# Kernel tuning notes

Hardware: AMD Instinct MI355X
Metric: run time of the kernel (lower is better)

## Reference

```python
import jax, jax.numpy as jnp
import numpy as np

THRESHOLD = 0.35      # overlap_thresh
NEGPOS_RATIO = 7
VAR0, VAR1 = 0.1, 0.2  # self.variance


def make_priors():
    # Standard RetinaFace 640x640 anchor grid -> 16800 priors (cx, cy, w, h)
    img = 640
    steps = [8, 16, 32]
    min_sizes = [[16, 32], [64, 128], [256, 512]]
    out = []
    for step, ms in zip(steps, min_sizes):
        f = img // step
        ii, jj = np.meshgrid(np.arange(f), np.arange(f), indexing="ij")
        cx = ((jj + 0.5) * step / img).ravel().astype(np.float32)
        cy = ((ii + 0.5) * step / img).ravel().astype(np.float32)
        for m in ms:
            s = np.full_like(cx, m / img)
            out.append(np.stack([cx, cy, s, s], axis=-1))
    return jnp.asarray(np.concatenate(out, axis=0), dtype=jnp.float32)


def jaccard(a, b):
    # a: [O,4] point-form gt boxes, b: [P,4] point-form priors -> IoU [O,P]
    lt = jnp.maximum(a[:, None, :2], b[None, :, :2])
    rb = jnp.minimum(a[:, None, 2:], b[None, :, 2:])
    wh = jnp.clip(rb - lt, 0.0)
    inter = wh[..., 0] * wh[..., 1]
    area_a = ((a[:, 2] - a[:, 0]) * (a[:, 3] - a[:, 1]))[:, None]
    area_b = ((b[:, 2] - b[:, 0]) * (b[:, 3] - b[:, 1]))[None, :]
    return inter / (area_a + area_b - inter)


def setup_inputs() -> dict:
    key = jax.random.key(0)
    ks = jax.random.split(key, 7)
    B, P, O = 64, 16800, 64
    loc_data = jax.random.normal(ks[0], (B, P, 4), jnp.float32)
    conf_data = jax.random.normal(ks[1], (B, P, 2), jnp.float32)
    landm_data = jax.random.normal(ks[2], (B, P, 10), jnp.float32)
    priors = make_priors()
    # targets: [B, O, 15] = [xmin ymin xmax ymax | 10 landmark coords | label]
    c = jax.random.uniform(ks[3], (B, O, 2), minval=0.15, maxval=0.85)
    wh = jax.random.uniform(ks[4], (B, O, 2), minval=0.05, maxval=0.3)
    boxes = jnp.concatenate([jnp.clip(c - wh / 2, 1e-3, 0.999),
                             jnp.clip(c + wh / 2, 1e-3, 0.999)], axis=-1)
    landms = jax.random.uniform(ks[5], (B, O, 10))
    lab = jnp.where(jax.random.uniform(ks[6], (B, O, 1)) < 0.8, 1.0, -1.0)
    targets = jnp.concatenate([boxes, landms, lab], axis=-1).astype(jnp.float32)
    return {"loc_data": loc_data, "conf_data": conf_data,
            "landm_data": landm_data, "priors": priors, "targets": targets}


def _smooth_l1(x):
    ax = jnp.abs(x)
    return jnp.where(ax < 1.0, 0.5 * ax * ax, ax - 0.5)


def reference(loc_data, conf_data, landm_data, priors, targets):
    B, P, C = conf_data.shape
    O = targets.shape[1]
    priors_pf = jnp.concatenate([priors[:, :2] - priors[:, 2:] * 0.5,
                                 priors[:, :2] + priors[:, 2:] * 0.5], axis=1)

    def match_one(t):
        truths = t[:, :4]
        landms = t[:, 4:14]
        labels = t[:, 14].astype(jnp.int32)
        ov = jaccard(truths, priors_pf)               # [O,P]
        bp_ov = ov.max(axis=1)                         # best prior per truth
        bp_idx = jnp.argmax(ov, axis=1)
        valid = bp_ov >= 0.2                           # RetinaFace gt filter
        bt_ov = ov.max(axis=0)                         # best truth per prior
        bt_idx = jnp.argmax(ov, axis=0)
        # index_fill_(best_prior_idx, 2) for valid gts, ensure best prior kept
        bt_ov = bt_ov.at[bp_idx].set(jnp.where(valid, 2.0, bt_ov[bp_idx]))
        bt_idx = bt_idx.at[bp_idx].set(jnp.arange(O))
        matched = truths[bt_idx]                       # [P,4] point form
        conf = labels[bt_idx]
        conf = jnp.where(bt_ov < THRESHOLD, 0, conf)
        # encode loc target
        g_cxcy = ((matched[:, :2] + matched[:, 2:]) * 0.5 - priors[:, :2]) / (VAR0 * priors[:, 2:])
        g_wh = jnp.log((matched[:, 2:] - matched[:, :2]) / priors[:, 2:]) / VAR1
        loc = jnp.concatenate([g_cxcy, g_wh], axis=1)
        # encode landmark target (5 points)
        ml = landms[bt_idx].reshape(P, 5, 2)
        lm = ((ml - priors[:, None, :2]) / (VAR0 * priors[:, None, 2:])).reshape(P, 10)
        any_valid = jnp.any(valid)                     # early-return branch of match()
        return (jnp.where(any_valid, loc, 0.0),
                jnp.where(any_valid, conf, 0),
                jnp.where(any_valid, lm, 0.0))

    loc_t, conf_t, landm_t = jax.vmap(match_one)(targets)
    loc_t = jax.lax.stop_gradient(loc_t)       # targets built from .data in torch
    landm_t = jax.lax.stop_gradient(landm_t)

    # landmark loss over conf_t > 0
    pos1 = conf_t > 0
    N1 = jnp.maximum(pos1.sum().astype(jnp.float32), 1.0)
    loss_landm = jnp.sum(jnp.where(pos1[..., None], _smooth_l1(landm_data - landm_t), 0.0))

    # localization loss over conf_t != 0 (labels -1 and 1 both positive)
    pos = conf_t != 0
    conf_t1 = jnp.where(pos, 1, conf_t)        # conf_t[pos] = 1 -> values in {0,1}
    loss_l = jnp.sum(jnp.where(pos[..., None], _smooth_l1(loc_data - loc_t), 0.0))

    # hard negative mining
    lse = jax.nn.logsumexp(conf_data, axis=2)                       # [B,P]
    picked = jnp.take_along_axis(conf_data, conf_t1[..., None], axis=2)[..., 0]
    ce_all = lse - picked                                            # per-anchor CE
    rank_score = jnp.where(pos, 0.0, ce_all)
    loss_idx = jnp.argsort(-rank_score, axis=1)
    idx_rank = jnp.argsort(loss_idx, axis=1)
    num_pos = pos.sum(axis=1, keepdims=True)
    num_neg = jnp.minimum(NEGPOS_RATIO * num_pos, P - 1)
    neg = idx_rank < num_neg
    union = pos | neg
    loss_c = jnp.sum(jnp.where(union, ce_all, 0.0))

    N = jnp.maximum(num_pos.sum().astype(jnp.float32), 1.0)
    return loss_l / N, loss_c / N, loss_landm / N1
```

## Files before the change

### kernel.cpp

```cpp
#include <hip/hip_runtime.h>
#include <math.h>

#define B 64
#define P 16800
#define O 64
#define THRESH 0.35f
#define VALID_T 0.2f
#define HB 2048
#define HSHIFT 21
#define AREA_M 0.34f
#define CCAP 4096
#define MULT 2
#define RPB 2
#define CHB (MULT * 256)
#define NB2 ((P + CHB - 1) / CHB)
#define KD1B ((B / RPB) * NB2)
#define KB2B (B * O / 4)

__device__ __forceinline__ float smooth_l1(float x) {
    float ax = fabsf(x);
    return ax < 1.f ? 0.5f * ax * ax : ax - 0.5f;
}
__device__ __forceinline__ float lse2(float c0, float c1) {
    float m = fmaxf(c0, c1);
    return m + __logf(__expf(c0 - m) + __expf(c1 - m));
}
__device__ __forceinline__ void iou_upd(float4 t, float area_a,
                                        float px1, float py1, float px2, float py2,
                                        float area_b,
                                        float& bnum, float& bden, int& bio, int o) {
    float w = fmaxf(fminf(t.z, px2) - fmaxf(t.x, px1), 0.f);
    float h = fmaxf(fminf(t.w, py2) - fmaxf(t.y, py1), 0.f);
    float inter = w * h;
    float den = area_a + area_b - inter;
    if (inter * bden > bnum * den) { bnum = inter; bden = den; bio = o; }
}
__device__ __forceinline__ float wave_sum(float v) {
#pragma unroll
    for (int s = 32; s > 0; s >>= 1) v += __shfl_down(v, s, 64);
    return v;
}
__device__ __forceinline__ int wave_sum_i(int v) {
#pragma unroll
    for (int s = 32; s > 0; s >>= 1) v += __shfl_down(v, s, 64);
    return v;
}
__device__ __forceinline__ float wave_min(float v) {
#pragma unroll
    for (int s = 32; s > 0; s >>= 1) v = fminf(v, __shfl_xor(v, s, 64));
    return v;
}
__device__ __forceinline__ float wave_max(float v) {
#pragma unroll
    for (int s = 32; s > 0; s >>= 1) v = fmaxf(v, __shfl_xor(v, s, 64));
    return v;
}
__device__ __forceinline__ int wave_sufscan(int v, int lane) {
#pragma unroll
    for (int s = 1; s < 64; s <<= 1) {
        int o = __shfl_down(v, s, 64);
        if (lane + s < 64) v += o;
    }
    return v;
}
__device__ __forceinline__ void wave0_select(const int* h, int nb, int k,
                                             int* s_bin, int* s_kk, int tid) {
    if (tid >= 64) return;
    int lane = tid;
    int bpl = (nb + 63) >> 6;
    int b0 = lane * bpl;
    int s = 0;
    for (int i = 0; i < bpl; ++i) { int bb = b0 + i; if (bb < nb) s += h[bb]; }
    int suf = wave_sufscan(s, lane);
    int sufn = __shfl_down(suf, 1, 64);
    if (lane == 63) sufn = 0;
    if (suf >= k && sufn < k) {
        int cum = sufn;
        for (int i = bpl - 1; i >= 0; --i) {
            int bb = b0 + i; if (bb >= nb) continue;
            int hv = h[bb];
            if (cum + hv >= k) { *s_bin = bb; *s_kk = k - cum; break; }
            cum += hv;
        }
    }
}

__global__ void __launch_bounds__(256) kMain(
        const float* __restrict__ loc_data,
        const float* __restrict__ landm_data, const float* __restrict__ priors,
        const float* __restrict__ targets,
        unsigned char* __restrict__ pflag,
        int* __restrict__ num_pos,
        float* __restrict__ gsum, int* __restrict__ np1_tot,
        unsigned long long* __restrict__ bp_final) {
    if (blockIdx.x >= KD1B) {
        int pair = (blockIdx.x - KD1B) * 4 + (threadIdx.x >> 6);
        int lane = threadIdx.x & 63;
        int o = pair & (O - 1);
        int b = pair >> 6;
        const float* tt = &targets[(b * O + o) * 15];
        float tx1 = tt[0], ty1 = tt[1], tx2 = tt[2], ty2 = tt[3];
        float area_a = (tx2 - tx1) * (ty2 - ty1);
        float4 tb = make_float4(tx1, ty1, tx2, ty2);
        float bn = 0.f, bd = 1.f;
        unsigned bp = 0u;
        const int fs[6]   = {80, 80, 40, 40, 20, 20};
        const int ms[6]   = {16, 32, 64, 128, 256, 512};
        const int base[6] = {0, 6400, 12800, 14400, 16000, 16400};
#pragma unroll
        for (int c = 0; c < 6; ++c) {
            int f = fs[c];
            float inv = (float)f;
            float h = (float)ms[c] * (0.5f / 640.f);
            int j0 = (int)floorf((tx1 - h) * inv - 0.5f) - 1; if (j0 < 0) j0 = 0;
            int j1 = (int)ceilf((tx2 + h) * inv - 0.5f) + 1;  if (j1 > f - 1) j1 = f - 1;
            int i0 = (int)floorf((ty1 - h) * inv - 0.5f) - 1; if (i0 < 0) i0 = 0;
            int i1 = (int)ceilf((ty2 + h) * inv - 0.5f) + 1;  if (i1 > f - 1) i1 = f - 1;
            if (j1 < j0 || i1 < i0) continue;
            int nj = j1 - j0 + 1;
            int n = (i1 - i0 + 1) * nj;
            float rcp_nj = 1.0f / (float)nj;
            for (int idx = lane; idx < n; idx += 64) {
                int ii = (int)((float)idx * rcp_nj);
                int jj = idx - ii * nj;
                if (jj < 0) { ii--; jj += nj; } else if (jj >= nj) { ii++; jj -= nj; }
                int p = base[c] + (i0 + ii) * f + (j0 + jj);
                float4 q = ((const float4*)priors)[p];
                float px1 = q.x - q.z * 0.5f, py1 = q.y - q.w * 0.5f;
                float px2 = q.x + q.z * 0.5f, py2 = q.y + q.w * 0.5f;
                float areab = (px2 - px1) * (py2 - py1);
                float w = fmaxf(fminf(tb.z, px2) - fmaxf(tb.x, px1), 0.f);
                float hh = fmaxf(fminf(tb.w, py2) - fmaxf(tb.y, py1), 0.f);
                float inter = w * hh;
                float den = area_a + areab - inter;
                float l = bn * den, r = inter * bd;
                if (r > l) { bn = inter; bd = den; bp = (unsigned)p; }
            }
        }
#pragma unroll
        for (int s = 32; s > 0; s >>= 1) {
            float no = __shfl_xor(bn, s, 64), dd = __shfl_xor(bd, s, 64);
            unsigned po = __shfl_xor(bp, s, 64);
            float l = bn * dd, r = no * bd;
            bool take = (r > l) || (r == l && po < bp);
            if (take) { bn = no; bd = dd; bp = po; }
        }
        if (lane == 0) {
            float iou = bn / bd;
            bp_final[b * O + o] = ((unsigned long long)__float_as_uint(iou) << 32)
                                | (unsigned)(0xFFFFFFFFu - bp);
        }
        return;
    }
    int blk = blockIdx.x % NB2;
    int rp = blockIdx.x / NB2;
    int p0 = blk * CHB;
    __shared__ float traw[O * 15];
    __shared__ float4 t4[O];
    __shared__ float ta[O], lab[O];
    __shared__ float wredf[2][4];
    __shared__ int wredi[2][4];
    int tid = threadIdx.x;
    int wid = tid >> 6, lid = tid & 63;
    float px1[MULT], py1[MULT], px2[MULT], py2[MULT], areab[MULT];
    float4 pr4[MULT];
    bool act[MULT];
    float cbx1[MULT], cby1[MULT], cbx2[MULT], cby2[MULT], camn[MULT], camx[MULT];
#pragma unroll
    for (int mi = 0; mi < MULT; ++mi) {
        int p = p0 + mi * 256 + tid;
        act[mi] = (p < P);
        int pc = act[mi] ? p : (P - 1);
        float4 q = ((const float4*)priors)[pc];
        pr4[mi] = q;
        px1[mi] = q.x - q.z * 0.5f; py1[mi] = q.y - q.w * 0.5f;
        px2[mi] = q.x + q.z * 0.5f; py2[mi] = q.y + q.w * 0.5f;
        areab[mi] = (px2[mi] - px1[mi]) * (py2[mi] - py1[mi]);
        cbx1[mi] = wave_min(px1[mi]); cby1[mi] = wave_min(py1[mi]);
        cbx2[mi] = wave_max(px2[mi]); cby2[mi] = wave_max(py2[mi]);
        camn[mi] = wave_min(areab[mi]); camx[mi] = wave_max(areab[mi]);
    }
    for (int r = 0; r < RPB; ++r) {
        int b = rp * RPB + r;
        __syncthreads();
        if (tid < O * 15 / 4)
            ((float4*)traw)[tid] = ((const float4*)(targets + (size_t)b * O * 15))[tid];
        __syncthreads();
        if (tid < 64) {
            const float* tr = &traw[tid * 15];
            float a0 = tr[0], a1 = tr[1], a2 = tr[2], a3 = tr[3];
            t4[tid] = make_float4(a0, a1, a2, a3);
            ta[tid] = (a2 - a0) * (a3 - a1);
            lab[tid] = tr[14];
        }
        __syncthreads();
        float4 tl = t4[lid];
        float Aal = ta[lid];
        unsigned long long mk[MULT];
#pragma unroll
        for (int mi = 0; mi < MULT; ++mi) {
            bool pass = (fminf(tl.z, cbx2[mi]) - fmaxf(tl.x, cbx1[mi]) > 0.f) &&
                        (fminf(tl.w, cby2[mi]) - fmaxf(tl.y, cby1[mi]) > 0.f) &&
                        (Aal >= AREA_M * camn[mi]) && (camx[mi] >= AREA_M * Aal);
            mk[mi] = __ballot(pass);
        }
        float bnum[MULT], bden[MULT]; int bi[MULT];
#pragma unroll
        for (int mi = 0; mi < MULT; ++mi) {
            bnum[mi] = 0.f; bden[mi] = 1.f; bi[mi] = 0;
            unsigned long long mm = mk[mi];
            float Ap = areab[mi];
            while (mm) {
                int o = __ffsll(mm) - 1;
                mm &= mm - 1;
                float4 t = t4[o];
                float Aa = ta[o];
                if (Aa >= AREA_M * Ap && Ap >= AREA_M * Aa)
                    iou_upd(t, Aa, px1[mi], py1[mi], px2[mi], py2[mi], Ap,
                            bnum[mi], bden[mi], bi[mi], o);
            }
        }
        float ll = 0.f, llm = 0.f;
        int cp = 0, cp1 = 0;
#pragma unroll
        for (int mi = 0; mi < MULT; ++mi) {
            if (!act[mi]) continue;
            int p = p0 + mi * 256 + tid;
            float best = bnum[mi] / bden[mi];
            int conf = (best >= THRESH) ? (int)lab[bi[mi]] : 0;
            bool pos = conf != 0;
            pflag[(size_t)b * P + p] = pos ? 1 : 0;
            if (pos) {
                cp++;
                int ti = bi[mi];
                float cx = pr4[mi].x, cy = pr4[mi].y, sw = pr4[mi].z, sh = pr4[mi].w;
                float4 t = t4[ti];
                float gx = ((t.x + t.z) * 0.5f - cx) / (0.1f * sw);
                float gy = ((t.y + t.w) * 0.5f - cy) / (0.1f * sh);
                float gw = logf((t.z - t.x) / sw) / 0.2f;
                float gh = logf((t.w - t.y) / sh) / 0.2f;
                const float* ld = &loc_data[(size_t)(b * P + p) * 4];
                ll += smooth_l1(ld[0] - gx) + smooth_l1(ld[1] - gy) +
                      smooth_l1(ld[2] - gw) + smooth_l1(ld[3] - gh);
                if (conf > 0) {
                    cp1++;
                    const float* lmd = &landm_data[(size_t)(b * P + p) * 10];
                    const float* lmt = &traw[ti * 15 + 4];
                    for (int k5 = 0; k5 < 5; ++k5) {
                        float lx = (lmt[k5 * 2 + 0] - cx) / (0.1f * sw);
                        float ly = (lmt[k5 * 2 + 1] - cy) / (0.1f * sh);
                        llm += smooth_l1(lmd[k5 * 2 + 0] - lx) + smooth_l1(lmd[k5 * 2 + 1] - ly);
                    }
                }
            }
        }
        float s_ll = wave_sum(ll), s_llm = wave_sum(llm);
        int s_cp = wave_sum_i(cp), s_cp1 = wave_sum_i(cp1);
        if (lid == 0) {
            wredf[0][wid] = s_ll; wredf[1][wid] = s_llm;
            wredi[0][wid] = s_cp; wredi[1][wid] = s_cp1;
        }
        __syncthreads();
        if (tid == 0) {
            float ll_t = wredf[0][0] + wredf[0][1] + wredf[0][2] + wredf[0][3];
            float llm_t = wredf[1][0] + wredf[1][1] + wredf[1][2] + wredf[1][3];
            int cp_t = wredi[0][0] + wredi[0][1] + wredi[0][2] + wredi[0][3];
            int cp1_t = wredi[1][0] + wredi[1][1] + wredi[1][2] + wredi[1][3];
            if (ll_t != 0.f)  atomicAdd(&gsum[0], ll_t);
            if (llm_t != 0.f) atomicAdd(&gsum[1], llm_t);
            if (cp_t)  atomicAdd(&num_pos[b], cp_t);
            if (cp1_t) atomicAdd(np1_tot, cp1_t);
        }
    }
}

__global__ void __launch_bounds__(1024) kTail(
        const float* __restrict__ priors, const float* __restrict__ targets,
        const float* __restrict__ loc_data, const float* __restrict__ conf_data,
        const float* __restrict__ landm_data,
        const unsigned long long* __restrict__ bp_final,
        const unsigned char* __restrict__ pflag,
        const int* __restrict__ num_pos,
        float* __restrict__ gsum, int* __restrict__ np1_tot, int* __restrict__ np_tot,
        float* __restrict__ lossc_tot, int* __restrict__ done,
        float* __restrict__ out) {
    __shared__ __align__(16) unsigned lrow[P];
    __shared__ int lh4[4][HB];
    __shared__ float4 t4[O];
    __shared__ float ta[O], lab[O];
    __shared__ int sp[O];
    __shared__ int hist2[256];
    __shared__ unsigned lcand[CCAP];
    __shared__ int s_np, s_bin0, s_kk0, s_bin, s_kk, s_cnt;
    __shared__ float wredf[16];
    __shared__ int wredi[16];
    __shared__ float s_cepw[16];
    __shared__ float s_sumgt;
    int* lh = lh4[0];

    int b = blockIdx.x;
    int tid = threadIdx.x;
    for (int i = tid; i < 4 * HB; i += 1024) lh4[0][i] = 0;
    if (tid == 0) s_cnt = 0;
    int p = 0, v = 0;
    if (tid < O) {
        const float* tt = &targets[(b * O + tid) * 15];
        float4 tj = make_float4(tt[0], tt[1], tt[2], tt[3]);
        t4[tid] = tj;
        ta[tid] = (tj.z - tj.x) * (tj.w - tj.y);
        lab[tid] = tt[14];
        unsigned long long kpk = bp_final[b * O + tid];
        p = (int)(0xFFFFFFFFu - (unsigned)(kpk & 0xFFFFFFFFu));
        float iou = __uint_as_float((unsigned)(kpk >> 32));
        v = (iou >= VALID_T) ? 1 : 0;
        sp[tid] = p;
    }
    __syncthreads();
    const float4* c4 = (const float4*)(conf_data + (size_t)b * P * 2);
    const uchar4* f4v = (const uchar4*)(pflag + (size_t)b * P);
    int* lhm = lh4[tid >> 8];
    float cep = 0.f;
    for (int i = tid; i < P / 4; i += 1024) {
        float4 a = c4[2 * i];
        float4 c = c4[2 * i + 1];
        uchar4 fl = f4v[i];
        float l0 = lse2(a.x, a.y), l1 = lse2(a.z, a.w);
        float l2 = lse2(c.x, c.y), l3 = lse2(c.z, c.w);
        bool q0 = fl.x != 0, q1 = fl.y != 0, q2 = fl.z != 0, q3 = fl.w != 0;
        float ce0 = l0 - (q0 ? a.y : a.x);
        float ce1 = l1 - (q1 ? a.w : a.z);
        float ce2 = l2 - (q2 ? c.y : c.x);
        float ce3 = l3 - (q3 ? c.w : c.z);
        if (q0) cep += ce0;
        if (q1) cep += ce1;
        if (q2) cep += ce2;
        if (q3) cep += ce3;
        unsigned u0 = __float_as_uint(q0 ? 0.f : ce0);
        unsigned u1 = __float_as_uint(q1 ? 0.f : ce1);
        unsigned u2 = __float_as_uint(q2 ? 0.f : ce2);
        unsigned u3 = __float_as_uint(q3 ? 0.f : ce3);
        ((uint4*)lrow)[i] = make_uint4(u0, u1, u2, u3);
        atomicAdd(&lhm[u0 >> HSHIFT], 1);
        atomicAdd(&lhm[u1 >> HSHIFT], 1);
        atomicAdd(&lhm[u2 >> HSHIFT], 1);
        atomicAdd(&lhm[u3 >> HSHIFT], 1);
    }
    {
        float sc = wave_sum(cep);
        if ((tid & 63) == 0) s_cepw[tid >> 6] = sc;
    }
    __syncthreads();
    for (int i = tid; i < HB; i += 1024)
        lh[i] = lh4[0][i] + lh4[1][i] + lh4[2][i] + lh4[3][i];
    __syncthreads();
    int dnp = 0, dn1 = 0;
    float dll = 0.f, dllm = 0.f, dce = 0.f;
    if (tid < O) {
        int j = tid;
        bool winner = true;
        for (int jj = j + 1; jj < O; ++jj)
            if (sp[jj] == p) { winner = false; break; }
        if (winner) {
            float4 q = ((const float4*)priors)[p];
            float px1 = q.x - q.z * 0.5f, py1 = q.y - q.w * 0.5f;
            float px2 = q.x + q.z * 0.5f, py2 = q.y + q.w * 0.5f;
            float areab = (px2 - px1) * (py2 - py1);
            float bnum = 0.f, bden = 1.f; int bi = 0;
            for (int o = 0; o < O; ++o) {
                float Aa = ta[o];
                if (Aa >= AREA_M * areab && areab >= AREA_M * Aa)
                    iou_upd(t4[o], Aa, px1, py1, px2, py2, areab, bnum, bden, bi, o);
            }
            float best = bnum / bden;
            float ov_new = v ? 2.0f : best;
            int conf_old = (best >= THRESH) ? (int)lab[bi] : 0;
            int conf_new = (ov_new >= THRESH) ? (int)lab[j] : 0;
            float2 c01 = ((const float2*)conf_data)[b * P + p];
            float c0 = c01.x, c1 = c01.y;
            float lse = lse2(c0, c1);
            bool po = conf_old != 0, pn = conf_new != 0;
            float ceo = lse - (po ? c1 : c0), cen = lse - (pn ? c1 : c0);
            float rvo = po ? 0.f : ceo, rvn = pn ? 0.f : cen;
            if (__float_as_uint(rvo) != __float_as_uint(rvn)) {
                lrow[p] = __float_as_uint(rvn);
                int bo = __float_as_uint(rvo) >> HSHIFT, bn = __float_as_uint(rvn) >> HSHIFT;
                if (bo != bn) { atomicAdd(&lh[bn], 1); atomicAdd(&lh[bo], -1); }
            }
            const float* ld = &loc_data[(size_t)(b * P + p) * 4];
            auto enc_ll = [&](int ti) -> float {
                float4 t = t4[ti];
                float gx = ((t.x + t.z) * 0.5f - q.x) / (0.1f * q.z);
                float gy = ((t.y + t.w) * 0.5f - q.y) / (0.1f * q.w);
                float gw = logf((t.z - t.x) / q.z) / 0.2f;
                float gh = logf((t.w - t.y) / q.w) / 0.2f;
                return smooth_l1(ld[0] - gx) + smooth_l1(ld[1] - gy) +
                       smooth_l1(ld[2] - gw) + smooth_l1(ld[3] - gh);
            };
            if (po) dll -= enc_ll(bi);
            if (pn) dll += enc_ll(j);
            dce = (pn ? cen : 0.f) - (po ? ceo : 0.f);
            dnp = (int)pn - (int)po;
            const float* lmd = &landm_data[(size_t)(b * P + p) * 10];
            auto enc_lm = [&](int ti) -> float {
                const float* lmt = &targets[(b * O + ti) * 15 + 4];
                float sum = 0.f;
                for (int k5 = 0; k5 < 5; ++k5) {
                    float lx = (lmt[k5 * 2 + 0] - q.x) / (0.1f * q.z);
                    float ly = (lmt[k5 * 2 + 1] - q.y) / (0.1f * q.w);
                    sum += smooth_l1(lmd[k5 * 2 + 0] - lx) + smooth_l1(lmd[k5 * 2 + 1] - ly);
                }
                return sum;
            };
            if (conf_old > 0) dllm -= enc_lm(bi);
            if (conf_new > 0) dllm += enc_lm(j);
            dn1 = (int)(conf_new > 0) - (int)(conf_old > 0);
        }
    }
    float pce_reg = 0.f;
    if (tid < 64) {
        float r_ll = wave_sum(dll), r_lm = wave_sum(dllm), r_ce = wave_sum(dce);
        int r_np = wave_sum_i(dnp), r_n1 = wave_sum_i(dn1);
        if (tid == 0) {
            if (r_ll != 0.f) atomicAdd(&gsum[0], r_ll);
            if (r_lm != 0.f) atomicAdd(&gsum[1], r_lm);
            float cep_tot = 0.f;
            for (int i = 0; i < 16; ++i) cep_tot += s_cepw[i];
            pce_reg = cep_tot + r_ce;
            int np = num_pos[b] + r_np;
            s_np = np;
            atomicAdd(np_tot, np);
            if (r_n1) atomicAdd(np1_tot, r_n1);
        }
    }
    __syncthreads();
    int k = s_np * 7;
    if (k > P - 1) k = P - 1;
    if (tid == 0) { s_bin0 = (k <= 0) ? -1 : 0; s_kk0 = (k <= 0) ? 0 : k; }
    if (k > 0) wave0_select(lh, HB, k, &s_bin0, &s_kk0, tid);
    __syncthreads();
    int bin = s_bin0;
    int kk0 = s_kk0;
    float topk_b = 0.f;
    if (bin >= 0) {
        if (tid < 256) hist2[tid] = 0;
        __syncthreads();
        unsigned lo_bound = ((unsigned)(bin + 1)) << HSHIFT;
        float sumgt = 0.f;
        for (int i = tid; i < P / 4; i += 1024) {
            uint4 u4 = ((const uint4*)lrow)[i];
#define TAIL_H(u) { if ((u) >= lo_bound) sumgt += __uint_as_float(u); \
                    else if (((u) >> HSHIFT) == (unsigned)bin) { \
                        int idx = atomicAdd(&s_cnt, 1); \
                        if (idx < CCAP) lcand[idx] = (u); \
                        atomicAdd(&hist2[((u) >> 13) & 255], 1); } }
            TAIL_H(u4.x) TAIL_H(u4.y) TAIL_H(u4.z) TAIL_H(u4.w)
#undef TAIL_H
        }
        float sg = wave_sum(sumgt);
        if ((tid & 63) == 0) wredf[tid >> 6] = sg;
        __syncthreads();
        if (tid == 0) {
            float t = 0.f;
            for (int i = 0; i < 16; ++i) t += wredf[i];
            s_sumgt = t;
        }
        wave0_select(hist2, 256, kk0, &s_bin, &s_kk, tid);
        __syncthreads();
        unsigned pref = (((unsigned)bin) << HSHIFT) | (((unsigned)s_bin) << 13);
        unsigned resolved = (0xFFFFFFFFu << HSHIFT) | (255u << 13);
        int kk = s_kk;
        int m = s_cnt;
        bool useG = (m > CCAP);
        for (int pass = 0; pass < 2; ++pass) {
            int sh = pass == 0 ? 5 : 0;
            int nb = pass == 0 ? 256 : 32;
            if (tid < nb) hist2[tid] = 0;
            __syncthreads();
            if (!useG) {
                for (int i = tid; i < m; i += 1024) {
                    unsigned u = lcand[i];
                    if ((u & resolved) == pref) atomicAdd(&hist2[(u >> sh) & (nb - 1)], 1);
                }
            } else {
                for (int pp = tid; pp < P; pp += 1024) {
                    unsigned u = lrow[pp];
                    if ((u & resolved) == pref) atomicAdd(&hist2[(u >> sh) & (nb - 1)], 1);
                }
            }
            __syncthreads();
            wave0_select(hist2, nb, kk, &s_bin, &s_kk, tid);
            __syncthreads();
            pref |= ((unsigned)s_bin) << sh;
            resolved |= (unsigned)(nb - 1) << sh;
            kk = s_kk;
        }
        float tv = __uint_as_float(pref);
        float sumS = 0.f; int cntS = 0;
        for (int pp = tid; pp < P; pp += 1024) {
            unsigned u = lrow[pp];
            if ((u >> HSHIFT) == (unsigned)bin) {
                float val = __uint_as_float(u);
                if (val > tv) { sumS += val; cntS++; }
            }
        }
        float s2 = wave_sum(sumS); int c2 = wave_sum_i(cntS);
        if ((tid & 63) == 0) { wredf[tid >> 6] = s2; wredi[tid >> 6] = c2; }
        __syncthreads();
        if (tid == 0) {
            float st = 0.f; int ct = 0;
            for (int i = 0; i < 16; ++i) { st += wredf[i]; ct += wredi[i]; }
            topk_b = s_sumgt + st + (float)(kk0 - ct) * tv;
        }
    }
    if (tid == 0) {
        atomicAdd(lossc_tot, pce_reg + topk_b);
        __threadfence();
        int old = atomicAdd(done, 1);
        if (old == B - 1) {
            float g0 = atomicAdd(&gsum[0], 0.f);
            float g1 = atomicAdd(&gsum[1], 0.f);
            float lc = atomicAdd(lossc_tot, 0.f);
            int np = atomicAdd(np_tot, 0);
            int n1 = atomicAdd(np1_tot, 0);
            float N = fmaxf((float)np, 1.f);
            float N1 = fmaxf((float)n1, 1.f);
            out[0] = g0 / N;
            out[1] = lc / N;
            out[2] = g1 / N1;
        }
    }
}

extern "C" void kernel_launch(void* const* d_in, const int* in_sizes, int n_in,
                              void* d_out, int out_size, void* d_ws, size_t ws_size,
                              hipStream_t stream) {
    const float* loc_data   = (const float*)d_in[0];
    const float* conf_data  = (const float*)d_in[1];
    const float* landm_data = (const float*)d_in[2];
    const float* priors     = (const float*)d_in[3];
    const float* targets    = (const float*)d_in[4];
    float* out = (float*)d_out;

    char* ws = (char*)d_ws;
    size_t off = 0;
    auto alloc = [&](size_t bytes) -> void* {
        void* pp = ws + off;
        off += (bytes + 255) & ~(size_t)255;
        return pp;
    };
    unsigned char* pflag = (unsigned char*)alloc((size_t)B * P);
    unsigned long long* bp_final = (unsigned long long*)alloc((size_t)B * O * 8);
    size_t acc_bytes = (size_t)(B * 4 + 64);
    char* acc = (char*)alloc(acc_bytes);
    int*   num_pos      = (int*)acc;
    float* gsum         = (float*)(acc + B * 4);
    int*   np1_tot      = (int*)(acc + B * 4 + 8);
    int*   np_tot       = (int*)(acc + B * 4 + 12);
    float* lossc_tot    = (float*)(acc + B * 4 + 16);
    int*   done         = (int*)(acc + B * 4 + 20);

    hipMemsetAsync(acc, 0, acc_bytes, stream);
    kMain<<<dim3(KD1B + KB2B), dim3(256), 0, stream>>>(loc_data, landm_data,
                                                       priors, targets, pflag,
                                                       num_pos, gsum, np1_tot,
                                                       bp_final);
    kTail<<<dim3(B), dim3(1024), 0, stream>>>(priors, targets, loc_data, conf_data,
                                              landm_data, bp_final, pflag,
                                              num_pos, gsum, np1_tot, np_tot,
                                              lossc_tot, done, out);
}
```

Baseline: 165.6 us.

## Move per-GT best-prior search into tail kernel and privatize tail histograms

The per-ground-truth best-prior IoU search moves out of extra blocks in the main kernel and into the start of the per-batch tail kernel. Each wave computes four GTs and writes the result to shared memory, so the global bp_final buffer and its round trip go away. The tail's candidate collection now uses wave-aggregated ballot atomics on the shared counter, and the radix-select histograms are split into four per-256-thread copies to reduce atomic contention. The trade-off is that the tail kernel, which runs only 64 blocks, now does the IoU search serially before its main work, which may lengthen the critical path.

```diff
diff --git a/kernel.cpp b/kernel.cpp
--- a/kernel.cpp
+++ b/kernel.cpp
@@ -15,7 +15,6 @@
 #define CHB (MULT * 256)
 #define NB2 ((P + CHB - 1) / CHB)
 #define KD1B ((B / RPB) * NB2)
-#define KB2B (B * O / 4)
 
 __device__ __forceinline__ float smooth_l1(float x) {
     float ax = fabsf(x);
@@ -91,67 +90,7 @@
         const float* __restrict__ targets,
         unsigned char* __restrict__ pflag,
         int* __restrict__ num_pos,
-        float* __restrict__ gsum, int* __restrict__ np1_tot,
-        unsigned long long* __restrict__ bp_final) {
-    if (blockIdx.x >= KD1B) {
-        int pair = (blockIdx.x - KD1B) * 4 + (threadIdx.x >> 6);
-        int lane = threadIdx.x & 63;
-        int o = pair & (O - 1);
-        int b = pair >> 6;
-        const float* tt = &targets[(b * O + o) * 15];
-        float tx1 = tt[0], ty1 = tt[1], tx2 = tt[2], ty2 = tt[3];
-        float area_a = (tx2 - tx1) * (ty2 - ty1);
-        float4 tb = make_float4(tx1, ty1, tx2, ty2);
-        float bn = 0.f, bd = 1.f;
-        unsigned bp = 0u;
-        const int fs[6]   = {80, 80, 40, 40, 20, 20};
-        const int ms[6]   = {16, 32, 64, 128, 256, 512};
-        const int base[6] = {0, 6400, 12800, 14400, 16000, 16400};
-#pragma unroll
-        for (int c = 0; c < 6; ++c) {
-            int f = fs[c];
-            float inv = (float)f;
-            float h = (float)ms[c] * (0.5f / 640.f);
-            int j0 = (int)floorf((tx1 - h) * inv - 0.5f) - 1; if (j0 < 0) j0 = 0;
-            int j1 = (int)ceilf((tx2 + h) * inv - 0.5f) + 1;  if (j1 > f - 1) j1 = f - 1;
-            int i0 = (int)floorf((ty1 - h) * inv - 0.5f) - 1; if (i0 < 0) i0 = 0;
-            int i1 = (int)ceilf((ty2 + h) * inv - 0.5f) + 1;  if (i1 > f - 1) i1 = f - 1;
-            if (j1 < j0 || i1 < i0) continue;
-            int nj = j1 - j0 + 1;
-            int n = (i1 - i0 + 1) * nj;
-            float rcp_nj = 1.0f / (float)nj;
-            for (int idx = lane; idx < n; idx += 64) {
-                int ii = (int)((float)idx * rcp_nj);
-                int jj = idx - ii * nj;
-                if (jj < 0) { ii--; jj += nj; } else if (jj >= nj) { ii++; jj -= nj; }
-                int p = base[c] + (i0 + ii) * f + (j0 + jj);
-                float4 q = ((const float4*)priors)[p];
-                float px1 = q.x - q.z * 0.5f, py1 = q.y - q.w * 0.5f;
-                float px2 = q.x + q.z * 0.5f, py2 = q.y + q.w * 0.5f;
-                float areab = (px2 - px1) * (py2 - py1);
-                float w = fmaxf(fminf(tb.z, px2) - fmaxf(tb.x, px1), 0.f);
-                float hh = fmaxf(fminf(tb.w, py2) - fmaxf(tb.y, py1), 0.f);
-                float inter = w * hh;
-                float den = area_a + areab - inter;
-                float l = bn * den, r = inter * bd;
-                if (r > l) { bn = inter; bd = den; bp = (unsigned)p; }
-            }
-        }
-#pragma unroll
-        for (int s = 32; s > 0; s >>= 1) {
-            float no = __shfl_xor(bn, s, 64), dd = __shfl_xor(bd, s, 64);
-            unsigned po = __shfl_xor(bp, s, 64);
-            float l = bn * dd, r = no * bd;
-            bool take = (r > l) || (r == l && po < bp);
-            if (take) { bn = no; bd = dd; bp = po; }
-        }
-        if (lane == 0) {
-            float iou = bn / bd;
-            bp_final[b * O + o] = ((unsigned long long)__float_as_uint(iou) << 32)
-                                | (unsigned)(0xFFFFFFFFu - bp);
-        }
-        return;
-    }
+        float* __restrict__ gsum, int* __restrict__ np1_tot) {
     int blk = blockIdx.x % NB2;
     int rp = blockIdx.x / NB2;
     int p0 = blk * CHB;
@@ -278,7 +217,6 @@
         const float* __restrict__ priors, const float* __restrict__ targets,
         const float* __restrict__ loc_data, const float* __restrict__ conf_data,
         const float* __restrict__ landm_data,
-        const unsigned long long* __restrict__ bp_final,
         const unsigned char* __restrict__ pflag,
         const int* __restrict__ num_pos,
         float* __restrict__ gsum, int* __restrict__ np1_tot, int* __restrict__ np_tot,
@@ -286,10 +224,12 @@
         float* __restrict__ out) {
     __shared__ __align__(16) unsigned lrow[P];
     __shared__ int lh4[4][HB];
+    __shared__ unsigned long long s_bpk[O];
     __shared__ float4 t4[O];
     __shared__ float ta[O], lab[O];
     __shared__ int sp[O];
     __shared__ int hist2[256];
+    __shared__ int hist2r[4][256];
     __shared__ unsigned lcand[CCAP];
     __shared__ int s_np, s_bin0, s_kk0, s_bin, s_kk, s_cnt;
     __shared__ float wredf[16];
@@ -300,8 +240,66 @@
 
     int b = blockIdx.x;
     int tid = threadIdx.x;
+    int lane = tid & 63;
+    int wv = tid >> 6;
     for (int i = tid; i < 4 * HB; i += 1024) lh4[0][i] = 0;
     if (tid == 0) s_cnt = 0;
+    for (int it = 0; it < 4; ++it) {
+        int o = wv + it * 16;
+        const float* tt = &targets[(b * O + o) * 15];
+        float tx1 = tt[0], ty1 = tt[1], tx2 = tt[2], ty2 = tt[3];
+        float area_a = (tx2 - tx1) * (ty2 - ty1);
+        float4 tb = make_float4(tx1, ty1, tx2, ty2);
+        float bn = 0.f, bd = 1.f;
+        unsigned bp = 0u;
+        const int fs[6]   = {80, 80, 40, 40, 20, 20};
+        const int ms[6]   = {16, 32, 64, 128, 256, 512};
+        const int base[6] = {0, 6400, 12800, 14400, 16000, 16400};
+#pragma unroll
+        for (int c = 0; c < 6; ++c) {
+            int f = fs[c];
+            float inv = (float)f;
+            float h = (float)ms[c] * (0.5f / 640.f);
+            int j0 = (int)floorf((tx1 - h) * inv - 0.5f) - 1; if (j0 < 0) j0 = 0;
+            int j1 = (int)ceilf((tx2 + h) * inv - 0.5f) + 1;  if (j1 > f - 1) j1 = f - 1;
+            int i0 = (int)floorf((ty1 - h) * inv - 0.5f) - 1; if (i0 < 0) i0 = 0;
+            int i1 = (int)ceilf((ty2 + h) * inv - 0.5f) + 1;  if (i1 > f - 1) i1 = f - 1;
+            if (j1 < j0 || i1 < i0) continue;
+            int nj = j1 - j0 + 1;
+            int n = (i1 - i0 + 1) * nj;
+            float rcp_nj = 1.0f / (float)nj;
+            for (int idx = lane; idx < n; idx += 64) {
+                int ii = (int)((float)idx * rcp_nj);
+                int jj = idx - ii * nj;
+                if (jj < 0) { ii--; jj += nj; } else if (jj >= nj) { ii++; jj -= nj; }
+                int p = base[c] + (i0 + ii) * f + (j0 + jj);
+                float4 q = ((const float4*)priors)[p];
+                float px1 = q.x - q.z * 0.5f, py1 = q.y - q.w * 0.5f;
+                float px2 = q.x + q.z * 0.5f, py2 = q.y + q.w * 0.5f;
+                float areab = (px2 - px1) * (py2 - py1);
+                float w = fmaxf(fminf(tb.z, px2) - fmaxf(tb.x, px1), 0.f);
+                float hh = fmaxf(fminf(tb.w, py2) - fmaxf(tb.y, py1), 0.f);
+                float inter = w * hh;
+                float den = area_a + areab - inter;
+                float l = bn * den, r = inter * bd;
+                if (r > l) { bn = inter; bd = den; bp = (unsigned)p; }
+            }
+        }
+#pragma unroll
+        for (int s = 32; s > 0; s >>= 1) {
+            float no = __shfl_xor(bn, s, 64), dd = __shfl_xor(bd, s, 64);
+            unsigned po = __shfl_xor(bp, s, 64);
+            float l = bn * dd, r = no * bd;
+            bool take = (r > l) || (r == l && po < bp);
+            if (take) { bn = no; bd = dd; bp = po; }
+        }
+        if (lane == 0) {
+            float iou = bn / bd;
+            s_bpk[o] = ((unsigned long long)__float_as_uint(iou) << 32)
+                     | (unsigned)(0xFFFFFFFFu - bp);
+        }
+    }
+    __syncthreads();
     int p = 0, v = 0;
     if (tid < O) {
         const float* tt = &targets[(b * O + tid) * 15];
@@ -309,13 +307,12 @@
         t4[tid] = tj;
         ta[tid] = (tj.z - tj.x) * (tj.w - tj.y);
         lab[tid] = tt[14];
-        unsigned long long kpk = bp_final[b * O + tid];
+        unsigned long long kpk = s_bpk[tid];
         p = (int)(0xFFFFFFFFu - (unsigned)(kpk & 0xFFFFFFFFu));
         float iou = __uint_as_float((unsigned)(kpk >> 32));
         v = (iou >= VALID_T) ? 1 : 0;
         sp[tid] = p;
     }
-    __syncthreads();
     const float4* c4 = (const float4*)(conf_data + (size_t)b * P * 2);
     const uchar4* f4v = (const uchar4*)(pflag + (size_t)b * P);
     int* lhm = lh4[tid >> 8];
@@ -347,7 +344,7 @@
     }
     {
         float sc = wave_sum(cep);
-        if ((tid & 63) == 0) s_cepw[tid >> 6] = sc;
+        if (lane == 0) s_cepw[wv] = sc;
     }
     __syncthreads();
     for (int i = tid; i < HB; i += 1024)
@@ -442,28 +439,45 @@
     int kk0 = s_kk0;
     float topk_b = 0.f;
     if (bin >= 0) {
-        if (tid < 256) hist2[tid] = 0;
+        for (int i = tid; i < 4 * 256; i += 1024) hist2r[0][i] = 0;
         __syncthreads();
         unsigned lo_bound = ((unsigned)(bin + 1)) << HSHIFT;
+        int* h2 = hist2r[tid >> 8];
         float sumgt = 0.f;
         for (int i = tid; i < P / 4; i += 1024) {
             uint4 u4 = ((const uint4*)lrow)[i];
-#define TAIL_H(u) { if ((u) >= lo_bound) sumgt += __uint_as_float(u); \
-                    else if (((u) >> HSHIFT) == (unsigned)bin) { \
-                        int idx = atomicAdd(&s_cnt, 1); \
-                        if (idx < CCAP) lcand[idx] = (u); \
-                        atomicAdd(&hist2[((u) >> 13) & 255], 1); } }
-            TAIL_H(u4.x) TAIL_H(u4.y) TAIL_H(u4.z) TAIL_H(u4.w)
-#undef TAIL_H
+#define TAIL_E(u) { \
+            bool gt = (u) >= lo_bound; \
+            bool inb = !gt && (((u) >> HSHIFT) == (unsigned)bin); \
+            if (gt) sumgt += __uint_as_float(u); \
+            unsigned long long mkb = __ballot(inb); \
+            if (mkb) { \
+                unsigned long long act = __ballot(true); \
+                int ldr = __ffsll(act) - 1; \
+                int cnt = __popcll(mkb); \
+                int bas = 0; \
+                if (lane == ldr) bas = atomicAdd(&s_cnt, cnt); \
+                bas = __shfl(bas, ldr, 64); \
+                if (inb) { \
+                    int pos = bas + __popcll(mkb & ((1ull << lane) - 1ull)); \
+                    if (pos < CCAP) lcand[pos] = (u); \
+                    atomicAdd(&h2[((u) >> 13) & 255], 1); \
+                } \
+            } }
+            TAIL_E(u4.x) TAIL_E(u4.y) TAIL_E(u4.z) TAIL_E(u4.w)
+#undef TAIL_E
         }
         float sg = wave_sum(sumgt);
-        if ((tid & 63) == 0) wredf[tid >> 6] = sg;
+        if (lane == 0) wredf[wv] = sg;
         __syncthreads();
         if (tid == 0) {
             float t = 0.f;
             for (int i = 0; i < 16; ++i) t += wredf[i];
             s_sumgt = t;
         }
+        if (tid < 256) hist2[tid] = hist2r[0][tid] + hist2r[1][tid] +
+                                    hist2r[2][tid] + hist2r[3][tid];
+        __syncthreads();
         wave0_select(hist2, 256, kk0, &s_bin, &s_kk, tid);
         __syncthreads();
         unsigned pref = (((unsigned)bin) << HSHIFT) | (((unsigned)s_bin) << 13);
@@ -474,19 +488,23 @@
         for (int pass = 0; pass < 2; ++pass) {
             int sh = pass == 0 ? 5 : 0;
             int nb = pass == 0 ? 256 : 32;
-            if (tid < nb) hist2[tid] = 0;
+            for (int i = tid; i < 4 * nb; i += 1024) hist2r[0][i] = 0;
             __syncthreads();
+            int* h2p = &hist2r[tid >> 8][0];
             if (!useG) {
                 for (int i = tid; i < m; i += 1024) {
                     unsigned u = lcand[i];
-                    if ((u & resolved) == pref) atomicAdd(&hist2[(u >> sh) & (nb - 1)], 1);
+                    if ((u & resolved) == pref) atomicAdd(&h2p[(u >> sh) & (nb - 1)], 1);
                 }
             } else {
                 for (int pp = tid; pp < P; pp += 1024) {
                     unsigned u = lrow[pp];
-                    if ((u & resolved) == pref) atomicAdd(&hist2[(u >> sh) & (nb - 1)], 1);
+                    if ((u & resolved) == pref) atomicAdd(&h2p[(u >> sh) & (nb - 1)], 1);
                 }
             }
+            __syncthreads();
+            if (tid < nb) hist2[tid] = hist2r[0][tid] + hist2r[1][tid] +
+                                       hist2r[2][tid] + hist2r[3][tid];
             __syncthreads();
             wave0_select(hist2, nb, kk, &s_bin, &s_kk, tid);
             __syncthreads();
@@ -504,7 +522,7 @@
             }
         }
         float s2 = wave_sum(sumS); int c2 = wave_sum_i(cntS);
-        if ((tid & 63) == 0) { wredf[tid >> 6] = s2; wredi[tid >> 6] = c2; }
+        if (lane == 0) { wredf[wv] = s2; wredi[wv] = c2; }
         __syncthreads();
         if (tid == 0) {
             float st = 0.f; int ct = 0;
@@ -549,7 +567,6 @@
         return pp;
     };
     unsigned char* pflag = (unsigned char*)alloc((size_t)B * P);
-    unsigned long long* bp_final = (unsigned long long*)alloc((size_t)B * O * 8);
     size_t acc_bytes = (size_t)(B * 4 + 64);
     char* acc = (char*)alloc(acc_bytes);
     int*   num_pos      = (int*)acc;
@@ -560,12 +577,11 @@
     int*   done         = (int*)(acc + B * 4 + 20);
 
     hipMemsetAsync(acc, 0, acc_bytes, stream);
-    kMain<<<dim3(KD1B + KB2B), dim3(256), 0, stream>>>(loc_data, landm_data,
-                                                       priors, targets, pflag,
-                                                       num_pos, gsum, np1_tot,
-                                                       bp_final);
+    kMain<<<dim3(KD1B), dim3(256), 0, stream>>>(loc_data, landm_data,
+                                                priors, targets, pflag,
+                                                num_pos, gsum, np1_tot);
     kTail<<<dim3(B), dim3(1024), 0, stream>>>(priors, targets, loc_data, conf_data,
-                                              landm_data, bp_final, pflag,
+                                              landm_data, pflag,
                                               num_pos, gsum, np1_tot, np_tot,
                                               lossc_tot, done, out);
 }
```

Measured after the change: 222.8 us. +34.6%, slower.

## Precompute per-anchor CE and histogram in main kernel, fix up positives in tail

Applied to the files above, without the earlier changes.

Moves the per-anchor background cross-entropy computation and its radix histogram out of the 64-block tail kernel into 256 extra blocks of the wide main kernel. Results go to a global rank buffer and per-batch histogram. The tail then copies the rank row into shared memory and only corrects flagged positive anchors: it zeroes their entry, adjusts the histogram, and sums their positive CE. This spreads the conf pass over many more blocks, at the cost of an extra global write and read of the rank array (about 4 MB), a larger memset, and global histogram atomics.

```diff
diff --git a/kernel.cpp b/kernel.cpp
--- a/kernel.cpp
+++ b/kernel.cpp
@@ -15,7 +15,9 @@
 #define CHB (MULT * 256)
 #define NB2 ((P + CHB - 1) / CHB)
 #define KD1B ((B / RPB) * NB2)
+#define KCEB (B * 4)
 #define KB2B (B * O / 4)
+#define QG (P / 4 / 4)
 
 __device__ __forceinline__ float smooth_l1(float x) {
     float ax = fabsf(x);
@@ -86,15 +88,16 @@
 }
 
 __global__ void __launch_bounds__(256) kMain(
-        const float* __restrict__ loc_data,
+        const float* __restrict__ loc_data, const float* __restrict__ conf_data,
         const float* __restrict__ landm_data, const float* __restrict__ priors,
         const float* __restrict__ targets,
-        unsigned char* __restrict__ pflag,
+        unsigned char* __restrict__ pflag, float* __restrict__ rank,
+        int* __restrict__ hist,
         int* __restrict__ num_pos,
         float* __restrict__ gsum, int* __restrict__ np1_tot,
         unsigned long long* __restrict__ bp_final) {
-    if (blockIdx.x >= KD1B) {
-        int pair = (blockIdx.x - KD1B) * 4 + (threadIdx.x >> 6);
+    if (blockIdx.x >= KD1B + KCEB) {
+        int pair = (blockIdx.x - KD1B - KCEB) * 4 + (threadIdx.x >> 6);
         int lane = threadIdx.x & 63;
         int o = pair & (O - 1);
         int b = pair >> 6;
@@ -149,6 +152,37 @@
             float iou = bn / bd;
             bp_final[b * O + o] = ((unsigned long long)__float_as_uint(iou) << 32)
                                 | (unsigned)(0xFFFFFFFFu - bp);
+        }
+        return;
+    }
+    if (blockIdx.x >= KD1B) {
+        int cb = blockIdx.x - KD1B;
+        int b = cb >> 2, q = cb & 3;
+        __shared__ int lhist[HB];
+        int tid = threadIdx.x;
+        for (int i = tid; i < HB; i += 256) lhist[i] = 0;
+        __syncthreads();
+        const float4* c4 = (const float4*)(conf_data + (size_t)b * P * 2);
+        uint4* r4 = (uint4*)(rank + (size_t)b * P);
+        for (int i = tid; i < QG; i += 256) {
+            int e = q * QG + i;
+            float4 a = c4[2 * e];
+            float4 c = c4[2 * e + 1];
+            unsigned u0 = __float_as_uint(lse2(a.x, a.y) - a.x);
+            unsigned u1 = __float_as_uint(lse2(a.z, a.w) - a.z);
+            unsigned u2 = __float_as_uint(lse2(c.x, c.y) - c.x);
+            unsigned u3 = __float_as_uint(lse2(c.z, c.w) - c.z);
+            r4[e] = make_uint4(u0, u1, u2, u3);
+            atomicAdd(&lhist[u0 >> HSHIFT], 1);
+            atomicAdd(&lhist[u1 >> HSHIFT], 1);
+            atomicAdd(&lhist[u2 >> HSHIFT], 1);
+            atomicAdd(&lhist[u3 >> HSHIFT], 1);
+        }
+        __syncthreads();
+        int* gh = hist + (size_t)b * HB;
+        for (int i = tid; i < HB; i += 256) {
+            int cgt = lhist[i];
+            if (cgt) atomicAdd(&gh[i], cgt);
         }
         return;
     }
@@ -280,12 +314,13 @@
         const float* __restrict__ landm_data,
         const unsigned long long* __restrict__ bp_final,
         const unsigned char* __restrict__ pflag,
+        const float* __restrict__ rank, const int* __restrict__ hist,
         const int* __restrict__ num_pos,
         float* __restrict__ gsum, int* __restrict__ np1_tot, int* __restrict__ np_tot,
         float* __restrict__ lossc_tot, int* __restrict__ done,
         float* __restrict__ out) {
     __shared__ __align__(16) unsigned lrow[P];
-    __shared__ int lh4[4][HB];
+    __shared__ int lh[HB];
     __shared__ float4 t4[O];
     __shared__ float ta[O], lab[O];
     __shared__ int sp[O];
@@ -296,11 +331,12 @@
     __shared__ int wredi[16];
     __shared__ float s_cepw[16];
     __shared__ float s_sumgt;
-    int* lh = lh4[0];
 
     int b = blockIdx.x;
     int tid = threadIdx.x;
-    for (int i = tid; i < 4 * HB; i += 1024) lh4[0][i] = 0;
+    int lane = tid & 63;
+    int wv = tid >> 6;
+    for (int i = tid; i < HB; i += 1024) lh[i] = hist[(size_t)b * HB + i];
     if (tid == 0) s_cnt = 0;
     int p = 0, v = 0;
     if (tid < O) {
@@ -315,43 +351,34 @@
         v = (iou >= VALID_T) ? 1 : 0;
         sp[tid] = p;
     }
+    const uint4* r4 = (const uint4*)(rank + (size_t)b * P);
+    for (int i = tid; i < P / 4; i += 1024) ((uint4*)lrow)[i] = r4[i];
     __syncthreads();
-    const float4* c4 = (const float4*)(conf_data + (size_t)b * P * 2);
     const uchar4* f4v = (const uchar4*)(pflag + (size_t)b * P);
-    int* lhm = lh4[tid >> 8];
+    const float2* cf2 = (const float2*)(conf_data + (size_t)b * P * 2);
     float cep = 0.f;
     for (int i = tid; i < P / 4; i += 1024) {
-        float4 a = c4[2 * i];
-        float4 c = c4[2 * i + 1];
         uchar4 fl = f4v[i];
-        float l0 = lse2(a.x, a.y), l1 = lse2(a.z, a.w);
-        float l2 = lse2(c.x, c.y), l3 = lse2(c.z, c.w);
-        bool q0 = fl.x != 0, q1 = fl.y != 0, q2 = fl.z != 0, q3 = fl.w != 0;
-        float ce0 = l0 - (q0 ? a.y : a.x);
-        float ce1 = l1 - (q1 ? a.w : a.z);
-        float ce2 = l2 - (q2 ? c.y : c.x);
-        float ce3 = l3 - (q3 ? c.w : c.z);
-        if (q0) cep += ce0;
-        if (q1) cep += ce1;
-        if (q2) cep += ce2;
-        if (q3) cep += ce3;
-        unsigned u0 = __float_as_uint(q0 ? 0.f : ce0);
-        unsigned u1 = __float_as_uint(q1 ? 0.f : ce1);
-        unsigned u2 = __float_as_uint(q2 ? 0.f : ce2);
-        unsigned u3 = __float_as_uint(q3 ? 0.f : ce3);
-        ((uint4*)lrow)[i] = make_uint4(u0, u1, u2, u3);
-        atomicAdd(&lhm[u0 >> HSHIFT], 1);
-        atomicAdd(&lhm[u1 >> HSHIFT], 1);
-        atomicAdd(&lhm[u2 >> HSHIFT], 1);
-        atomicAdd(&lhm[u3 >> HSHIFT], 1);
+        if (fl.x | fl.y | fl.z | fl.w) {
+#pragma unroll
+            for (int kq = 0; kq < 4; ++kq) {
+                unsigned char f = (kq == 0) ? fl.x : (kq == 1) ? fl.y : (kq == 2) ? fl.z : fl.w;
+                if (f) {
+                    int pp = i * 4 + kq;
+                    unsigned old = lrow[pp];
+                    lrow[pp] = 0u;
+                    atomicAdd(&lh[old >> HSHIFT], -1);
+                    atomicAdd(&lh[0], 1);
+                    float2 cc = cf2[pp];
+                    cep += lse2(cc.x, cc.y) - cc.y;
+                }
+            }
+        }
     }
     {
         float sc = wave_sum(cep);
-        if ((tid & 63) == 0) s_cepw[tid >> 6] = sc;
-    }
-    __syncthreads();
-    for (int i = tid; i < HB; i += 1024)
-        lh[i] = lh4[0][i] + lh4[1][i] + lh4[2][i] + lh4[3][i];
+        if (lane == 0) s_cepw[wv] = sc;
+    }
     __syncthreads();
     int dnp = 0, dn1 = 0;
     float dll = 0.f, dllm = 0.f, dce = 0.f;
@@ -457,7 +484,7 @@
 #undef TAIL_H
         }
         float sg = wave_sum(sumgt);
-        if ((tid & 63) == 0) wredf[tid >> 6] = sg;
+        if (lane == 0) wredf[wv] = sg;
         __syncthreads();
         if (tid == 0) {
             float t = 0.f;
@@ -504,7 +531,7 @@
             }
         }
         float s2 = wave_sum(sumS); int c2 = wave_sum_i(cntS);
-        if ((tid & 63) == 0) { wredf[tid >> 6] = s2; wredi[tid >> 6] = c2; }
+        if (lane == 0) { wredf[wv] = s2; wredi[wv] = c2; }
         __syncthreads();
         if (tid == 0) {
             float st = 0.f; int ct = 0;
@@ -548,8 +575,12 @@
         off += (bytes + 255) & ~(size_t)255;
         return pp;
     };
+    float* rank     = (float*)alloc((size_t)B * P * 4);
     unsigned char* pflag = (unsigned char*)alloc((size_t)B * P);
     unsigned long long* bp_final = (unsigned long long*)alloc((size_t)B * O * 8);
+    size_t hist_bytes = (size_t)B * HB * 4;
+    char* zbase = (char*)alloc(hist_bytes);
+    int* hist = (int*)zbase;
     size_t acc_bytes = (size_t)(B * 4 + 64);
     char* acc = (char*)alloc(acc_bytes);
     int*   num_pos      = (int*)acc;
@@ -558,14 +589,14 @@
     int*   np_tot       = (int*)(acc + B * 4 + 12);
     float* lossc_tot    = (float*)(acc + B * 4 + 16);
     int*   done         = (int*)(acc + B * 4 + 20);
-
-    hipMemsetAsync(acc, 0, acc_bytes, stream);
-    kMain<<<dim3(KD1B + KB2B), dim3(256), 0, stream>>>(loc_data, landm_data,
-                                                       priors, targets, pflag,
-                                                       num_pos, gsum, np1_tot,
-                                                       bp_final);
+    size_t zlen = (size_t)((acc + acc_bytes) - zbase);
+
+    hipMemsetAsync(zbase, 0, zlen, stream);
+    kMain<<<dim3(KD1B + KCEB + KB2B), dim3(256), 0, stream>>>(
+        loc_data, conf_data, landm_data, priors, targets,
+        pflag, rank, hist, num_pos, gsum, np1_tot, bp_final);
     kTail<<<dim3(B), dim3(1024), 0, stream>>>(priors, targets, loc_data, conf_data,
-                                              landm_data, bp_final, pflag,
+                                              landm_data, bp_final, pflag, rank, hist,
                                               num_pos, gsum, np1_tot, np_tot,
                                               lossc_tot, done, out);
 }
```

Result: no change. 168.1 us (+1.5%).
